# Performance work log

Measured on AMD Instinct MI355X. Metric: run time of the kernel, lower is better.

## Reference

```python
import jax
import jax.numpy as jnp
from jax import lax
import numpy as np

INPUT_DIM = 784
HIDDEN_DIM = 1024
BATCH = 256
N_BINS = 10


def setup_inputs() -> dict:
    key = jax.random.key(0)
    k1, k2, k3, k4, k5 = jax.random.split(key, 5)
    # kaiming-normal-ish init scales (faithful in spirit; exact values irrelevant for math)
    W = jax.random.normal(k1, (HIDDEN_DIM, INPUT_DIM), dtype=jnp.float32) * np.sqrt(2.0 / INPUT_DIM)
    c = jnp.zeros((HIDDEN_DIM, 1), dtype=jnp.float32)
    V = jax.random.normal(k2, (INPUT_DIM, HIDDEN_DIM, N_BINS), dtype=jnp.float32) * np.sqrt(2.0 / N_BINS)
    b = jnp.zeros((INPUT_DIM, N_BINS), dtype=jnp.float32)
    x = jax.random.randint(k3, (BATCH, INPUT_DIM), 0, N_BINS, dtype=jnp.int32)
    return {"x": x, "W": W, "c": c, "V": V, "b": b}


def reference(x, W, c, V, b):
    # x: [B, D] int pixel bins; W: [H, D]; c: [H, 1]; V: [D, H, 10]; b: [D, 10]
    B = x.shape[0]
    xf = x.astype(jnp.float32)  # [B, D]
    a0 = jnp.broadcast_to(c[:, 0][None, :], (B, W.shape[0]))  # [B, H]

    def step(a, inp):
        Vi, bi, Wi, xi = inp  # Vi:[H,10], bi:[10], Wi:[H], xi:[B]
        h = jax.nn.sigmoid(a)                       # [B, H]
        p = jax.nn.softmax(h @ Vi + bi, axis=1)     # [B, 10]
        a = a + xi[:, None] * Wi[None, :]           # rank-1 update, matches x_i @ W[:,i].T
        return a, p

    _, p_seq = lax.scan(step, a0, (V, b, W.T, xf.T))  # p_seq: [D, B, 10]
    p_hat = jnp.transpose(p_seq, (1, 2, 0))            # [B, 10, D] == torch.stack(p_hat, dim=2)
    return p_hat
```

## Files before the change

kernel.cpp:

```cpp
#include <hip/hip_runtime.h>
#include <stdint.h>

#define D_DIM 784
#define H_DIM 1024
#define B_DIM 256
#define NBIN  10
#define G_CH  16
#define T_CH  49
#define BT    16
#define LOG2E 1.4426950408889634f

#define VPREP_BLKS D_DIM
#define WPREP_BLKS 208

typedef _Float16 half8_t  __attribute__((ext_vector_type(8)));
typedef __fp16   fp16x2_t __attribute__((ext_vector_type(2)));
typedef float    float4_t __attribute__((ext_vector_type(4)));

__global__ void k_prep(const float* __restrict__ W, const float* __restrict__ V,
                       _Float16* __restrict__ Wt2h, _Float16* __restrict__ VB) {
    __shared__ __align__(16) float smem[5120];
    int tid = threadIdx.x;
    int bx  = blockIdx.x;

    if (bx < VPREP_BLKS) {
        int i = bx;
        const float4* src = (const float4*)(V + (size_t)i * H_DIM * NBIN);
        uint4* dst = (uint4*)VB + (size_t)i * 2048;
        #pragma unroll
        for (int p = 0; p < 2; ++p) {
            if (p) __syncthreads();
            #pragma unroll
            for (int qv = 0; qv < 5; ++qv) {
                float4 v = src[p * 1280 + qv * 256 + tid];
                *((float4*)&smem[(qv * 256 + tid) * 4]) = v;
            }
            __syncthreads();
            #pragma unroll
            for (int qv = 0; qv < 4; ++qv) {
                int pair = p * 1024 + qv * 256 + tid;
                int kk = pair >> 6, ll = pair & 63;
                int n = ll & 15, hb = kk * 32 + ((ll >> 4) & 3) * 8;
                union { _Float16 hh[8]; uint4 u; } o;
                #pragma unroll
                for (int jj = 0; jj < 8; ++jj)
                    o.hh[jj] = (_Float16)((n < NBIN) ? smem[(hb + jj) * NBIN + n - p * 5120] : 0.0f);
                dst[pair] = o.u;
            }
        }
    } else {
        int qw = bx - VPREP_BLKS;
        int j0 = (qw % 13) * 64, h0 = (qw / 13) * 64;
        float (*t)[65] = (float(*)[65])smem;
        int tj = tid & 63, tr = tid >> 6;
        int j = j0 + tj;
        #pragma unroll
        for (int r = 0; r < 16; ++r) {
            int hh = tr * 16 + r;
            t[hh][tj] = (j < D_DIM) ? W[(size_t)(h0 + hh) * D_DIM + j] : 0.0f;
        }
        __syncthreads();
        #pragma unroll
        for (int r = 0; r < 16; ++r) {
            int jj = tr * 16 + r;
            int jo = j0 + jj;
            if (jo < D_DIM) Wt2h[(size_t)jo * H_DIM + h0 + tj] = (_Float16)(t[tj][jj] * LOG2E);
        }
    }
}

__global__ __launch_bounds__(256)
void k_pscan(const _Float16* __restrict__ Wt2h, const int* __restrict__ x,
             const float* __restrict__ c, _Float16* __restrict__ PA) {
    int b   = blockIdx.x;
    int hg  = blockIdx.y;
    int tid = threadIdx.x;
    int hcol = hg * 256 + tid;
    int h0   = hcol * 2;

    __shared__ float xs[D_DIM];
    if (tid < D_DIM / 4) {
        int4 xi = ((const int4*)(x + (size_t)b * D_DIM))[tid];
        *((float4*)&xs[tid * 4]) =
            make_float4((float)xi.x, (float)xi.y, (float)xi.z, (float)xi.w);
    }
    float acc0 = c[h0] * LOG2E, acc1 = c[h0 + 1] * LOG2E;
    __syncthreads();

    const uint* wp  = (const uint*)Wt2h;
    uint*       pau = (uint*)PA;

    uint wvA[16], wvB[16];
    auto ldrow = [&](int t, uint (&wv)[16]) {
        #pragma unroll
        for (int r = 0; r < 16; ++r)
            wv[r] = wp[(size_t)(t * 16 + r) * 512 + hcol];
    };
    auto emit = [&](int t) {
        union { _Float16 hh[2]; uint u; } uu;
        uu.hh[0] = (_Float16)acc0; uu.hh[1] = (_Float16)acc1;
        pau[((size_t)t * B_DIM + b) * 512 + hcol] = uu.u;
    };
    auto fmas = [&](int t, const uint (&wv)[16]) {
        #pragma unroll
        for (int r = 0; r < 16; ++r) {
            union { uint u; _Float16 hh[2]; } uu; uu.u = wv[r];
            float xf = xs[t * 16 + r];
            acc0 += xf * (float)uu.hh[0];
            acc1 += xf * (float)uu.hh[1];
        }
    };

    ldrow(0, wvA);
    for (int t = 0; t < T_CH - 1; t += 2) {
        ldrow(t + 1, wvB);
        emit(t);     fmas(t, wvA);
        ldrow(t + 2, wvA);
        emit(t + 1); fmas(t + 1, wvB);
    }
    emit(T_CH - 1);
}

__global__ __launch_bounds__(256, 3)
void k_main(const _Float16* __restrict__ VB, const _Float16* __restrict__ Wt2h,
            const _Float16* __restrict__ PA, const int* __restrict__ x,
            const float* __restrict__ bias, float* __restrict__ out) {
    int bid = blockIdx.x;
    int lb  = (bid & 7) * 98 + (bid >> 3);
    int tc  = lb >> 4;
    int bt  = lb & 15;
    int tid = threadIdx.x;
    int w   = tid >> 6;
    int l   = tid & 63;
    int bl  = l & 15;
    int kg  = l >> 4;
    int bg  = bt * BT + bl;
    int i0  = tc * G_CH;

    __shared__ float red[2][4][64][17];
    __shared__ float bs[G_CH][16];

    {
        int ii = tid >> 4, n = tid & 15;
        bs[ii][n] = (n < NBIN) ? bias[(size_t)(i0 + ii) * NBIN + n] : 0.0f;
    }

    float a[8][8];
    {
        const _Float16* src = PA + ((size_t)tc * B_DIM + bg) * H_DIM + w * 256 + kg * 8;
        #pragma unroll
        for (int m = 0; m < 8; ++m) {
            half8_t av = *((const half8_t*)(src + m * 32));
            #pragma unroll
            for (int j = 0; j < 8; ++j) a[m][j] = (float)av[j];
        }
    }

    const int4* xp = (const int4*)(x + (size_t)bg * D_DIM + i0);

    const uint4* vp = (const uint4*)VB + ((size_t)i0 * 32 + w * 8) * 64 + l;
    uint4 vbuf[4];
    vbuf[0] = vp[0];
    vbuf[1] = vp[64];
    const uint4* vpr = vp + 128;

    const _Float16* whp = Wt2h + (size_t)i0 * H_DIM + w * 256 + kg * 8;
    half8_t whbuf[2];
    whbuf[0] = *((const half8_t*)whp);
    whbuf[1] = *((const half8_t*)(whp + 32));
    const _Float16* whr = whp + 64;

    float4_t acc = {0.f, 0.f, 0.f, 0.f};

    auto softmax_store = [&](int q) {
        const int buf = q & 1;
        float p4[4];
        #pragma unroll
        for (int qq = 0; qq < 4; ++qq) {
            float tot = red[buf][0][l][qq * 4 + w] + red[buf][1][l][qq * 4 + w]
                      + red[buf][2][l][qq * 4 + w] + red[buf][3][l][qq * 4 + w];
            float v = (bl < NBIN) ? tot + bs[q * 4 + qq][bl] : -3.0e38f;
            float vm = v;
            vm = fmaxf(vm, __shfl_xor(vm, 1));
            vm = fmaxf(vm, __shfl_xor(vm, 2));
            vm = fmaxf(vm, __shfl_xor(vm, 4));
            vm = fmaxf(vm, __shfl_xor(vm, 8));
            float e = __builtin_amdgcn_exp2f((v - vm) * LOG2E);
            float ss = e;
            ss += __shfl_xor(ss, 1); ss += __shfl_xor(ss, 2);
            ss += __shfl_xor(ss, 4); ss += __shfl_xor(ss, 8);
            p4[qq] = e * __builtin_amdgcn_rcpf(ss);
        }
        if (bl < NBIN) {
            int b = bt * BT + kg * 4 + w;
            size_t base = ((size_t)b * NBIN + bl) * D_DIM + i0 + q * 4;
            *((float4*)(out + base)) = make_float4(p4[0], p4[1], p4[2], p4[3]);
        }
    };

    for (int q = 0; q < 4; ++q) {
        int4 xi = xp[q];
        float xq0 = (float)xi.x, xq1 = (float)xi.y, xq2 = (float)xi.z, xq3 = (float)xi.w;
        #pragma unroll
        for (int s = 0; s < 32; ++s) {
            const int iis = s >> 3;
            const int m   = s & 7;
            const int nn  = q * 32 + s + 2;
            half8_t wh = whbuf[s & 1];
            if (nn < 128) {
                vbuf[(s + 2) & 3] = *vpr;
                whbuf[s & 1] = *((const half8_t*)whr);
                vpr += (((s + 3) & 7) == 0) ? 1600 : 64;
                whr += (((s + 3) & 7) == 0) ? 800  : 32;
            }
            union { half8_t h8; uint u32[4]; } af;
            #pragma unroll
            for (int p = 0; p < 4; ++p) {
                float s0 = __builtin_amdgcn_rcpf(1.0f + __builtin_amdgcn_exp2f(-a[m][2 * p]));
                float s1 = __builtin_amdgcn_rcpf(1.0f + __builtin_amdgcn_exp2f(-a[m][2 * p + 1]));
                union { fp16x2_t v; uint u; } cv;
                cv.v = __builtin_amdgcn_cvt_pkrtz(s0, s1);
                af.u32[p] = cv.u;
            }
            union { half8_t h8; uint4 u; } bf;
            bf.u = vbuf[s & 3];
            acc = __builtin_amdgcn_mfma_f32_16x16x32_f16(af.h8, bf.h8, acc, 0, 0, 0);
            float xf = (iis == 0) ? xq0 : (iis == 1) ? xq1 : (iis == 2) ? xq2 : xq3;
            a[m][0] += xf * (float)wh[0]; a[m][1] += xf * (float)wh[1];
            a[m][2] += xf * (float)wh[2]; a[m][3] += xf * (float)wh[3];
            a[m][4] += xf * (float)wh[4]; a[m][5] += xf * (float)wh[5];
            a[m][6] += xf * (float)wh[6]; a[m][7] += xf * (float)wh[7];
            if (m == 7) {
                float* rp = &red[q & 1][w][l][iis * 4];
                rp[0] = acc[0]; rp[1] = acc[1]; rp[2] = acc[2]; rp[3] = acc[3];
                acc = (float4_t){0.f, 0.f, 0.f, 0.f};
            }
        }
        __syncthreads();
        softmax_store(q);
    }
}

extern "C" void kernel_launch(void* const* d_in, const int* in_sizes, int n_in,
                              void* d_out, int out_size, void* d_ws, size_t ws_size,
                              hipStream_t stream) {
    const int*   x    = (const int*)d_in[0];
    const float* W    = (const float*)d_in[1];
    const float* c    = (const float*)d_in[2];
    const float* V    = (const float*)d_in[3];
    const float* bias = (const float*)d_in[4];
    float* out = (float*)d_out;

    char* ws = (char*)d_ws;
    size_t off = 0;
    _Float16* Wt2h = (_Float16*)(ws + off);
    off += (size_t)D_DIM * H_DIM * sizeof(_Float16);
    off = (off + 255) & ~(size_t)255;
    _Float16* VB = (_Float16*)(ws + off);
    off += (size_t)D_DIM * 32 * 64 * 8 * sizeof(_Float16);
    off = (off + 255) & ~(size_t)255;
    _Float16* PA = (_Float16*)(ws + off);

    k_prep<<<dim3(VPREP_BLKS + WPREP_BLKS), 256, 0, stream>>>(W, V, Wt2h, VB);
    k_pscan<<<dim3(B_DIM, 2), 256, 0, stream>>>(Wt2h, x, c, PA);
    k_main<<<dim3(D_DIM), 256, 0, stream>>>(VB, Wt2h, PA, x, bias, out);
}
```

Baseline: 204.4 us.

## Split each main block's 16-step chunk into two 8-step halves across 512 threads

Measured after the change: 240.3 us. +17.6%, slower.

```diff
diff --git a/kernel.cpp b/kernel.cpp
--- a/kernel.cpp
+++ b/kernel.cpp
@@ -7,6 +7,8 @@
 #define NBIN  10
 #define G_CH  16
 #define T_CH  49
+#define P_CH  8
+#define T_PS  98
 #define BT    16
 #define LOG2E 1.4426950408889634f
 
@@ -90,38 +92,37 @@
     const uint* wp  = (const uint*)Wt2h;
     uint*       pau = (uint*)PA;
 
-    uint wvA[16], wvB[16];
-    auto ldrow = [&](int t, uint (&wv)[16]) {
-        #pragma unroll
-        for (int r = 0; r < 16; ++r)
-            wv[r] = wp[(size_t)(t * 16 + r) * 512 + hcol];
+    uint wvA[8], wvB[8];
+    auto ldrow = [&](int t, uint (&wv)[8]) {
+        #pragma unroll
+        for (int r = 0; r < 8; ++r)
+            wv[r] = wp[(size_t)(t * 8 + r) * 512 + hcol];
     };
     auto emit = [&](int t) {
         union { _Float16 hh[2]; uint u; } uu;
         uu.hh[0] = (_Float16)acc0; uu.hh[1] = (_Float16)acc1;
         pau[((size_t)t * B_DIM + b) * 512 + hcol] = uu.u;
     };
-    auto fmas = [&](int t, const uint (&wv)[16]) {
-        #pragma unroll
-        for (int r = 0; r < 16; ++r) {
+    auto fmas = [&](int t, const uint (&wv)[8]) {
+        #pragma unroll
+        for (int r = 0; r < 8; ++r) {
             union { uint u; _Float16 hh[2]; } uu; uu.u = wv[r];
-            float xf = xs[t * 16 + r];
+            float xf = xs[t * 8 + r];
             acc0 += xf * (float)uu.hh[0];
             acc1 += xf * (float)uu.hh[1];
         }
     };
 
     ldrow(0, wvA);
-    for (int t = 0; t < T_CH - 1; t += 2) {
+    for (int t = 0; t < T_PS; t += 2) {
         ldrow(t + 1, wvB);
         emit(t);     fmas(t, wvA);
-        ldrow(t + 2, wvA);
+        if (t + 2 < T_PS) ldrow(t + 2, wvA);
         emit(t + 1); fmas(t + 1, wvB);
     }
-    emit(T_CH - 1);
-}
-
-__global__ __launch_bounds__(256, 3)
+}
+
+__global__ __launch_bounds__(512, 4)
 void k_main(const _Float16* __restrict__ VB, const _Float16* __restrict__ Wt2h,
             const _Float16* __restrict__ PA, const int* __restrict__ x,
             const float* __restrict__ bias, float* __restrict__ out) {
@@ -130,24 +131,29 @@
     int tc  = lb >> 4;
     int bt  = lb & 15;
     int tid = threadIdx.x;
-    int w   = tid >> 6;
+    int g   = tid >> 8;
+    int w   = (tid >> 6) & 3;
     int l   = tid & 63;
     int bl  = l & 15;
     int kg  = l >> 4;
     int bg  = bt * BT + bl;
-    int i0  = tc * G_CH;
+    int ib  = tc * G_CH;
+    int i0  = ib + g * P_CH;
 
     __shared__ float red[2][4][64][17];
     __shared__ float bs[G_CH][16];
 
     {
-        int ii = tid >> 4, n = tid & 15;
-        bs[ii][n] = (n < NBIN) ? bias[(size_t)(i0 + ii) * NBIN + n] : 0.0f;
+        if (tid < 256) {
+            int ii = tid >> 4, n = tid & 15;
+            bs[ii][n] = (n < NBIN) ? bias[(size_t)(ib + ii) * NBIN + n] : 0.0f;
+        }
     }
 
     float a[8][8];
     {
-        const _Float16* src = PA + ((size_t)tc * B_DIM + bg) * H_DIM + w * 256 + kg * 8;
+        int ct = tc * 2 + g;
+        const _Float16* src = PA + ((size_t)ct * B_DIM + bg) * H_DIM + w * 256 + kg * 8;
         #pragma unroll
         for (int m = 0; m < 8; ++m) {
             half8_t av = *((const half8_t*)(src + m * 32));
@@ -173,13 +179,12 @@
     float4_t acc = {0.f, 0.f, 0.f, 0.f};
 
     auto softmax_store = [&](int q) {
-        const int buf = q & 1;
         float p4[4];
         #pragma unroll
         for (int qq = 0; qq < 4; ++qq) {
-            float tot = red[buf][0][l][qq * 4 + w] + red[buf][1][l][qq * 4 + w]
-                      + red[buf][2][l][qq * 4 + w] + red[buf][3][l][qq * 4 + w];
-            float v = (bl < NBIN) ? tot + bs[q * 4 + qq][bl] : -3.0e38f;
+            float tot = red[g][0][l][qq * 4 + w] + red[g][1][l][qq * 4 + w]
+                      + red[g][2][l][qq * 4 + w] + red[g][3][l][qq * 4 + w];
+            float v = (bl < NBIN) ? tot + bs[g * P_CH + q * 4 + qq][bl] : -3.0e38f;
             float vm = v;
             vm = fmaxf(vm, __shfl_xor(vm, 1));
             vm = fmaxf(vm, __shfl_xor(vm, 2));
@@ -198,7 +203,7 @@
         }
     };
 
-    for (int q = 0; q < 4; ++q) {
+    for (int q = 0; q < 2; ++q) {
         int4 xi = xp[q];
         float xq0 = (float)xi.x, xq1 = (float)xi.y, xq2 = (float)xi.z, xq3 = (float)xi.w;
         #pragma unroll
@@ -207,7 +212,7 @@
             const int m   = s & 7;
             const int nn  = q * 32 + s + 2;
             half8_t wh = whbuf[s & 1];
-            if (nn < 128) {
+            if (nn < 64) {
                 vbuf[(s + 2) & 3] = *vpr;
                 whbuf[s & 1] = *((const half8_t*)whr);
                 vpr += (((s + 3) & 7) == 0) ? 1600 : 64;
@@ -231,13 +236,14 @@
             a[m][4] += xf * (float)wh[4]; a[m][5] += xf * (float)wh[5];
             a[m][6] += xf * (float)wh[6]; a[m][7] += xf * (float)wh[7];
             if (m == 7) {
-                float* rp = &red[q & 1][w][l][iis * 4];
+                float* rp = &red[g][w][l][iis * 4];
                 rp[0] = acc[0]; rp[1] = acc[1]; rp[2] = acc[2]; rp[3] = acc[3];
                 acc = (float4_t){0.f, 0.f, 0.f, 0.f};
             }
         }
         __syncthreads();
         softmax_store(q);
+        if (q == 0) __syncthreads();
     }
 }
 
@@ -263,5 +269,5 @@
 
     k_prep<<<dim3(VPREP_BLKS + WPREP_BLKS), 256, 0, stream>>>(W, V, Wt2h, VB);
     k_pscan<<<dim3(B_DIM, 2), 256, 0, stream>>>(Wt2h, x, c, PA);
-    k_main<<<dim3(D_DIM), 256, 0, stream>>>(VB, Wt2h, PA, x, bias, out);
-}
+    k_main<<<dim3(D_DIM), 512, 0, stream>>>(VB, Wt2h, PA, x, bias, out);
+}
```
